# Optimization experiments

Measured on AMD Instinct MI355X. Metric: run time of the kernel, lower is better.

The kernel has to match this reference:

```python
import jax, jax.numpy as jnp
import numpy as np

B, G, P, D, H, QK, E, FF, TOPK = 32, 500, 500, 128, 8, 16, 8, 512, 2
SQRT_EMB = 11.313708498984761
LOGIT_CLIP = 10.0
EPS_CV = 1e-10
EPS_IN = 1e-5


def setup_inputs() -> dict:
    key = jax.random.key(0)
    ks = jax.random.split(key, 16)
    s = 0.05
    inp = {
        'graph': jax.random.normal(ks[0], (B, 1, D), jnp.float32),
        'capacity': jax.random.uniform(ks[1], (B, G), jnp.float32),
        'ninf_mask': jnp.zeros((B, G, P), jnp.float32),
        'encoded_nodes': jax.random.normal(ks[2], (B, P, D), jnp.float32),
        'Wq': jax.random.normal(ks[3], (D + 1, H * QK), jnp.float32) * s,
        'Wk': jax.random.normal(ks[4], (D, H * QK), jnp.float32) * s,
        'Wv': jax.random.normal(ks[5], (D, H * QK), jnp.float32) * s,
        'Wcomb': jax.random.normal(ks[6], (H * QK, D), jnp.float32) * s,
        'w_gate': jax.random.normal(ks[7], (D, E), jnp.float32) * s,
        'W1': jax.random.normal(ks[8], (E, D, FF), jnp.float32) * s,
        'b1': jnp.zeros((E, FF), jnp.float32),
        'W2': jax.random.normal(ks[9], (E, FF, D), jnp.float32) * s,
        'b2': jnp.zeros((E, D), jnp.float32),
        'norm_w': jnp.ones((D,), jnp.float32),
        'norm_b': jnp.zeros((D,), jnp.float32),
    }
    return inp


def _heads(x, h):
    b, n, _ = x.shape
    return x.reshape(b, n, h, -1).transpose(0, 2, 1, 3)  # [b,h,n,qk]


def reference(graph, capacity, ninf_mask, encoded_nodes, Wq, Wk, Wv, Wcomb,
              w_gate, W1, b1, W2, b2, norm_w, norm_b):
    # ---- set_kv ----
    k = _heads(encoded_nodes @ Wk, H)  # [B,H,P,QK]
    v = _heads(encoded_nodes @ Wv, H)

    # ---- query build ----
    input1 = jnp.broadcast_to(graph, (B, G, D))
    input_cat = jnp.concatenate([input1, capacity[:, :, None]], axis=2)  # [B,G,D+1]
    q = _heads(input_cat @ Wq, H)  # [B,H,G,QK]

    # ---- multi-head attention ----
    score = jnp.einsum('bhgq,bhpq->bhgp', q, k) / jnp.sqrt(jnp.float32(QK))
    score = score + ninf_mask[:, None, :, :]
    w = jax.nn.softmax(score, axis=3)
    out = jnp.einsum('bhgp,bhpq->bhgq', w, v)
    out_concat = out.transpose(0, 2, 1, 3).reshape(B, G, H * QK)
    mh_atten_out = out_concat @ Wcomb  # [B,G,D]

    # ---- MoE (top-k gating, eval mode) ----
    tokens = mh_atten_out.reshape(B * G, D)
    logits = tokens @ w_gate                     # [T,E]
    topv, topi = jax.lax.top_k(logits, TOPK)
    topg = jax.nn.softmax(topv, axis=-1)
    T = tokens.shape[0]
    gates = jnp.zeros((T, E), tokens.dtype).at[jnp.arange(T)[:, None], topi].set(topg)
    importance = gates.sum(axis=0)
    moed_loss = jnp.var(importance, ddof=1) / (jnp.mean(importance) ** 2 + EPS_CV)
    h = jax.nn.relu(jnp.einsum('td,edf->tef', tokens, W1) + b1)  # [T,E,FF]
    y = jnp.einsum('tef,efd->ted', h, W2) + b2                   # [T,E,D]
    moe_out = jnp.einsum('te,ted->td', gates, y).reshape(B, G, D)

    # ---- Add & InstanceNorm1d (normalize over group dim per channel) ----
    added = mh_atten_out + moe_out
    mu = jnp.mean(added, axis=1, keepdims=True)
    var = jnp.var(added, axis=1, keepdims=True)
    normed = (added - mu) * jax.lax.rsqrt(var + EPS_IN) * norm_w + norm_b

    # ---- single-head probs ----
    score2 = jnp.einsum('bgd,bpd->bgp', normed, encoded_nodes)
    score_clipped = LOGIT_CLIP * jnp.tanh(score2 / SQRT_EMB)
    probs = jax.nn.softmax(score_clipped + ninf_mask, axis=2)
    return probs, moed_loss
```

## Files before the change

kernel.cpp:

```cpp
#include <hip/hip_runtime.h>
#include <math.h>

#define NB 32
#define NG 500
#define NP 500
#define ND 128
#define NH 8
#define NQK 16
#define NE 8
#define NFF 512
#define NT 16000

typedef __attribute__((ext_vector_type(8))) short bf16x8;
typedef __attribute__((ext_vector_type(4))) float f32x4;

static __device__ __forceinline__ unsigned short f2bf(float f) {
  unsigned int u = __float_as_uint(f);
  unsigned int r = (u + 0x7FFFu + ((u >> 16) & 1u)) >> 16;
  return (unsigned short)r;
}
static __device__ __forceinline__ float bf2f(unsigned short h) {
  return __uint_as_float(((unsigned int)h) << 16);
}

__global__ __launch_bounds__(256) void k_kv(const float* __restrict__ enc,
                                            const float* __restrict__ Wk,
                                            const float* __restrict__ Wv,
                                            float* __restrict__ kbuf,
                                            float* __restrict__ vbuf) {
  int r0 = blockIdx.x * 32;
  int tid = threadIdx.x;
  __shared__ float encS[32][128];
  const float4* e4 = (const float4*)(enc + (size_t)r0 * 128);
  float4* s4 = (float4*)&encS[0][0];
#pragma unroll
  for (int i = 0; i < 4; i++) s4[tid + i * 256] = e4[tid + i * 256];
  __syncthreads();
  int cg = tid & 31, rg = tid >> 5;
  int c0 = cg * 8;
  const float* W0 = (c0 < 128) ? (Wk + c0) : (Wv + (c0 - 128));
  float acc[4][8] = {};
  for (int d = 0; d < 128; d++) {
    float a0 = encS[rg * 4 + 0][d];
    float a1 = encS[rg * 4 + 1][d];
    float a2 = encS[rg * 4 + 2][d];
    float a3 = encS[rg * 4 + 3][d];
    float4 wlo = *(const float4*)(W0 + d * 128);
    float4 whi = *(const float4*)(W0 + d * 128 + 4);
    float w[8] = {wlo.x, wlo.y, wlo.z, wlo.w, whi.x, whi.y, whi.z, whi.w};
#pragma unroll
    for (int j = 0; j < 8; j++) {
      acc[0][j] += a0 * w[j];
      acc[1][j] += a1 * w[j];
      acc[2][j] += a2 * w[j];
      acc[3][j] += a3 * w[j];
    }
  }
#pragma unroll
  for (int i = 0; i < 4; i++) {
    int r = r0 + rg * 4 + i;
    int b = r / 500;
    int p = r - b * 500;
    int cc = (c0 < 128) ? c0 : (c0 - 128);
    int h = cc >> 4, qk = cc & 15;
    float* dst = (c0 < 128 ? kbuf : vbuf) + ((size_t)(b * 8 + h) * 500 + p) * 16 + qk;
    *(float4*)dst = make_float4(acc[i][0], acc[i][1], acc[i][2], acc[i][3]);
    *(float4*)(dst + 4) = make_float4(acc[i][4], acc[i][5], acc[i][6], acc[i][7]);
  }
}

__global__ void k_graphq(const float* __restrict__ graph,
                         const float* __restrict__ Wq,
                         float* __restrict__ gq) {
  int b = blockIdx.x, j = threadIdx.x;
  float s = 0.f;
  for (int d = 0; d < 128; d++) s += graph[b * 128 + d] * Wq[d * 128 + j];
  gq[b * 128 + j] = s;
}

__global__ __launch_bounds__(256) void k_maskT(const float* __restrict__ mask,
                                               unsigned short* __restrict__ mT) {
  int b = blockIdx.z;
  int pt = blockIdx.x * 32, gt = blockIdx.y * 32;
  __shared__ float t[32][33];
  int tx = threadIdx.x & 31, ty = threadIdx.x >> 5;
#pragma unroll
  for (int i = 0; i < 32; i += 8) {
    int g = gt + ty + i, p = pt + tx;
    t[ty + i][tx] = (g < NG && p < NP) ? mask[((size_t)b * NG + g) * NP + p] : 0.f;
  }
  __syncthreads();
#pragma unroll
  for (int i = 0; i < 32; i += 8) {
    int p = pt + ty + i, g = gt + tx;
    if (p < NP && g < NG)
      mT[((size_t)b * NP + p) * NG + g] = f2bf(t[tx][ty + i]);
  }
}

__global__ __launch_bounds__(256) void k_encT(const float* __restrict__ enc,
                                              float* __restrict__ encT) {
  int b = blockIdx.z;
  int pt = blockIdx.x * 32, dt = blockIdx.y * 32;
  __shared__ float t[32][33];
  int tx = threadIdx.x & 31, ty = threadIdx.x >> 5;
#pragma unroll
  for (int i = 0; i < 32; i += 8) {
    int p = pt + ty + i, d = dt + tx;
    t[ty + i][tx] = (p < NP) ? enc[((size_t)b * NP + p) * ND + d] : 0.f;
  }
  __syncthreads();
#pragma unroll
  for (int i = 0; i < 32; i += 8) {
    int d = dt + ty + i, p = pt + tx;
    if (p < NP)
      encT[((size_t)b * ND + d) * NP + p] = t[tx][ty + i];
  }
}

__global__ __launch_bounds__(256) void k_attn(const float* __restrict__ kbuf,
                                              const float* __restrict__ vbuf,
                                              const float* __restrict__ capacity,
                                              const float* __restrict__ gq,
                                              const float* __restrict__ Wq,
                                              const unsigned short* __restrict__ mT,
                                              float* __restrict__ att) {
  int d = blockIdx.x;
  int xc = d & 7, kk = d >> 3;
  int b = ((kk >> 3) << 3) | xc;
  int h = kk & 7;
  int bh = b * 8 + h;
  int half = blockIdx.y;
  int tid = threadIdx.x;
  __shared__ float2 AB[NP];
  __shared__ float vsh[NP][16];
  const float4* vp = (const float4*)(vbuf + (size_t)bh * NP * 16);
  float4* v4 = (float4*)&vsh[0][0];
  for (int i = tid; i < NP * 4; i += 256) v4[i] = vp[i];
  float gqv[16], wql[16];
#pragma unroll
  for (int j = 0; j < 16; j++) {
    gqv[j] = gq[b * 128 + h * 16 + j];
    wql[j] = Wq[128 * 128 + h * 16 + j];
  }
  const float4* kp = (const float4*)(kbuf + (size_t)bh * NP * 16);
  for (int p = tid; p < NP; p += 256) {
    float4 k0 = kp[p * 4 + 0], k1 = kp[p * 4 + 1];
    float4 k2 = kp[p * 4 + 2], k3 = kp[p * 4 + 3];
    float kv[16] = {k0.x, k0.y, k0.z, k0.w, k1.x, k1.y, k1.z, k1.w,
                    k2.x, k2.y, k2.z, k2.w, k3.x, k3.y, k3.z, k3.w};
    float a = 0.f, bb = 0.f;
#pragma unroll
    for (int j = 0; j < 16; j++) { a += gqv[j] * kv[j]; bb += wql[j] * kv[j]; }
    AB[p] = make_float2(a * 0.25f, bb * 0.25f);
  }
  __syncthreads();
  if (tid < 250) {
    int g = half * 250 + tid;
    float cap = capacity[b * NG + g];
    float l = 0.f;
    float o[16] = {};
    const unsigned short* mTb = mT + (size_t)b * NP * NG + g;
    for (int p = 0; p < NP; p++) {
      float2 ab = AB[p];
      float mval = bf2f(mTb[(size_t)p * NG]);
      float e = __expf(fmaf(cap, ab.y, ab.x) + mval);
      l += e;
      const float4* vr = (const float4*)(&vsh[p][0]);
      float4 va = vr[0], vb = vr[1], vc = vr[2], vd = vr[3];
      o[0] += e * va.x;  o[1] += e * va.y;  o[2] += e * va.z;  o[3] += e * va.w;
      o[4] += e * vb.x;  o[5] += e * vb.y;  o[6] += e * vb.z;  o[7] += e * vb.w;
      o[8] += e * vc.x;  o[9] += e * vc.y;  o[10] += e * vc.z; o[11] += e * vc.w;
      o[12] += e * vd.x; o[13] += e * vd.y; o[14] += e * vd.z; o[15] += e * vd.w;
    }
    float inv = 1.f / l;
    float* orow = att + ((size_t)(b * NG + g)) * 128 + h * 16;
#pragma unroll
    for (int j = 0; j < 16; j++) orow[j] = o[j] * inv;
  }
}

__global__ __launch_bounds__(256) void k_comb(const float* __restrict__ att,
                                              const float* __restrict__ Wc,
                                              float* __restrict__ mh) {
  int r0 = blockIdx.x * 32;
  int tid = threadIdx.x;
  __shared__ float aS[32][130];
  for (int idx = tid; idx < 32 * 32; idx += 256) {
    int r = idx >> 5, dg = idx & 31;
    float4 v = ((const float4*)att)[(size_t)(r0 + r) * 32 + dg];
    aS[r][dg * 4 + 0] = v.x; aS[r][dg * 4 + 1] = v.y;
    aS[r][dg * 4 + 2] = v.z; aS[r][dg * 4 + 3] = v.w;
  }
  __syncthreads();
  int cg = tid & 15, rg = tid >> 4;
  float acc[2][8] = {};
  for (int d = 0; d < 128; d++) {
    float a0 = aS[rg * 2 + 0][d];
    float a1 = aS[rg * 2 + 1][d];
    float4 wlo = *(const float4*)(Wc + d * 128 + cg * 8);
    float4 whi = *(const float4*)(Wc + d * 128 + cg * 8 + 4);
    float w[8] = {wlo.x, wlo.y, wlo.z, wlo.w, whi.x, whi.y, whi.z, whi.w};
#pragma unroll
    for (int j = 0; j < 8; j++) {
      acc[0][j] += a0 * w[j];
      acc[1][j] += a1 * w[j];
    }
  }
#pragma unroll
  for (int i = 0; i < 2; i++) {
    float* dst = mh + (size_t)(r0 + rg * 2 + i) * 128 + cg * 8;
    *(float4*)dst = make_float4(acc[i][0], acc[i][1], acc[i][2], acc[i][3]);
    *(float4*)(dst + 4) = make_float4(acc[i][4], acc[i][5], acc[i][6], acc[i][7]);
  }
}

__global__ __launch_bounds__(256) void k_gate(const float* __restrict__ mh,
                                              const float* __restrict__ wg,
                                              int* __restrict__ tlist,
                                              float* __restrict__ glist,
                                              int* __restrict__ cnt,
                                              float* __restrict__ imp) {
  int t0 = blockIdx.x * 256;
  int tid = threadIdx.x;
  __shared__ float wgS[128 * 8];
  __shared__ int lcnt[8];
  __shared__ float limp[8];
  __shared__ int lbase[8];
  for (int i = tid; i < 1024; i += 256) wgS[i] = wg[i];
  if (tid < 8) { lcnt[tid] = 0; limp[tid] = 0.f; }
  __syncthreads();
  int t = t0 + tid;
  bool ok = (t < NT);
  int i0 = 0, i1 = 0, r0 = 0, r1 = 0;
  float g0 = 0.f, g1 = 0.f;
  if (ok) {
    float lg[8] = {};
    const float* row = mh + (size_t)t * ND;
    for (int d = 0; d < ND; d += 4) {
      float4 x4 = *(const float4*)(row + d);
      float xs[4] = {x4.x, x4.y, x4.z, x4.w};
#pragma unroll
      for (int u = 0; u < 4; u++)
#pragma unroll
        for (int k = 0; k < 8; k++) lg[k] += xs[u] * wgS[(d + u) * 8 + k];
    }
    float v0 = -1e30f, v1 = -1e30f;
#pragma unroll
    for (int k = 0; k < 8; k++) {
      float l = lg[k];
      if (l > v0) { v1 = v0; i1 = i0; v0 = l; i0 = k; }
      else if (l > v1) { v1 = l; i1 = k; }
    }
    float ex = __expf(v1 - v0);
    float den = 1.0f + ex;
    g0 = 1.0f / den; g1 = ex / den;
    atomicAdd(&limp[i0], g0);
    atomicAdd(&limp[i1], g1);
    r0 = atomicAdd(&lcnt[i0], 1);
    r1 = atomicAdd(&lcnt[i1], 1);
  }
  __syncthreads();
  if (tid < 8) {
    lbase[tid] = atomicAdd(&cnt[tid], lcnt[tid]);
    atomicAdd(&imp[tid], limp[tid]);
  }
  __syncthreads();
  if (ok) {
    int p0 = lbase[i0] + r0;
    tlist[i0 * NT + p0] = t; glist[i0 * NT + p0] = g0;
    int p1 = lbase[i1] + r1;
    tlist[i1 * NT + p1] = t; glist[i1 * NT + p1] = g1;
  }
}

__global__ __launch_bounds__(64) void k_wpack(const float* __restrict__ W1,
                                              const float* __restrict__ W2,
                                              unsigned short* __restrict__ w1h,
                                              unsigned short* __restrict__ w1l,
                                              unsigned short* __restrict__ w2h,
                                              unsigned short* __restrict__ w2l) {
  int bid = blockIdx.x;
  int e = bid >> 8;
  int t = bid & 255;
  int l = threadIdx.x;
  int kg = 4 * (l >> 4);
  if (t < 128) {
    int kt = t >> 5, nt = t & 31;
    const float* src = W1 + (size_t)e * 128 * 512;
    size_t base = ((((size_t)e * 4 + kt) * 32 + nt) * 64 + l) * 8;
    int n = nt * 16 + (l & 15);
#pragma unroll
    for (int j = 0; j < 8; j++) {
      int k = kt * 32 + kg + (j & 3) + ((j >> 2) << 4);
      float v = src[(size_t)k * 512 + n];
      unsigned short hi = f2bf(v);
      w1h[base + j] = hi;
      w1l[base + j] = f2bf(v - bf2f(hi));
    }
  } else {
    int tt = t - 128;
    int kt = tt >> 3, nt = tt & 7;
    const float* src = W2 + (size_t)e * 512 * 128;
    size_t base = ((((size_t)e * 16 + kt) * 8 + nt) * 64 + l) * 8;
    int n = nt * 16 + (l & 15);
#pragma unroll
    for (int j = 0; j < 8; j++) {
      int k = kt * 32 + kg + (j & 3) + ((j >> 2) << 4);
      float v = src[(size_t)k * 128 + n];
      unsigned short hi = f2bf(v);
      w2h[base + j] = hi;
      w2l[base + j] = f2bf(v - bf2f(hi));
    }
  }
}

__global__ __launch_bounds__(256) void k_moe(const float* __restrict__ mh,
                                             const unsigned short* __restrict__ w1h,
                                             const unsigned short* __restrict__ w1l,
                                             const unsigned short* __restrict__ w2h,
                                             const unsigned short* __restrict__ w2l,
                                             const float* __restrict__ b1,
                                             const float* __restrict__ b2,
                                             const int* __restrict__ tlist,
                                             const float* __restrict__ glist,
                                             const int* __restrict__ cnt,
                                             float* __restrict__ acc) {
  int e = blockIdx.y;
  int n = cnt[e];
  int t0 = blockIdx.x * 32;
  if (t0 >= n) return;
  int tid = threadIdx.x;
  int wq = tid >> 6;
  int l = tid & 63;
  __shared__ int rT[32];
  __shared__ float rG[32];
  __shared__ unsigned short hH[32][132];
  __shared__ unsigned short hL[32][132];
  if (tid < 32) {
    int ok = (t0 + tid) < n;
    rT[tid] = ok ? tlist[e * NT + t0 + tid] : -1;
    rG[tid] = ok ? glist[e * NT + t0 + tid] : 0.f;
  }
  __syncthreads();

  int kg = 4 * (l >> 4);
  bf16x8 Ah[2][4], Al[2][4];
#pragma unroll
  for (int m = 0; m < 2; m++) {
    int myrow = m * 16 + (l & 15);
    int mytok = rT[myrow];
#pragma unroll
    for (int kt = 0; kt < 4; kt++) {
      float v[8];
      if (mytok >= 0) {
        const float* row = mh + (size_t)mytok * ND + kt * 32 + kg;
        float4 a = *(const float4*)(row);
        float4 b = *(const float4*)(row + 16);
        v[0] = a.x; v[1] = a.y; v[2] = a.z; v[3] = a.w;
        v[4] = b.x; v[5] = b.y; v[6] = b.z; v[7] = b.w;
      } else {
#pragma unroll
        for (int j = 0; j < 8; j++) v[j] = 0.f;
      }
#pragma unroll
      for (int j = 0; j < 8; j++) {
        unsigned short hi = f2bf(v[j]);
        Ah[m][kt][j] = (short)hi;
        Al[m][kt][j] = (short)f2bf(v[j] - bf2f(hi));
      }
    }
  }

  f32x4 zero4 = {0.f, 0.f, 0.f, 0.f};
  f32x4 yB[2][2] = {{zero4, zero4}, {zero4, zero4}};

  for (int c = 0; c < 4; c++) {
    f32x4 accA[2][2] = {{zero4, zero4}, {zero4, zero4}};
#pragma unroll
    for (int kt = 0; kt < 4; kt++) {
      bf16x8 bh[2], bl[2];
#pragma unroll
      for (int nt = 0; nt < 2; nt++) {
        int ntg = c * 8 + wq * 2 + nt;
        size_t fo = ((((size_t)e * 4 + kt) * 32 + ntg) * 64 + l) * 8;
        bh[nt] = *(const bf16x8*)(w1h + fo);
        bl[nt] = *(const bf16x8*)(w1l + fo);
      }
#pragma unroll
      for (int nt = 0; nt < 2; nt++)
#pragma unroll
        for (int m = 0; m < 2; m++) {
          accA[m][nt] = __builtin_amdgcn_mfma_f32_16x16x32_bf16(Ah[m][kt], bh[nt], accA[m][nt], 0, 0, 0);
          accA[m][nt] = __builtin_amdgcn_mfma_f32_16x16x32_bf16(Ah[m][kt], bl[nt], accA[m][nt], 0, 0, 0);
          accA[m][nt] = __builtin_amdgcn_mfma_f32_16x16x32_bf16(Al[m][kt], bh[nt], accA[m][nt], 0, 0, 0);
        }
    }
    __syncthreads();
#pragma unroll
    for (int nt = 0; nt < 2; nt++) {
      int nloc = wq * 32 + nt * 16 + (l & 15);
      float bv = b1[e * NFF + c * 128 + nloc];
#pragma unroll
      for (int m = 0; m < 2; m++)
#pragma unroll
        for (int r = 0; r < 4; r++) {
          int row = m * 16 + (l >> 4) * 4 + r;
          float hv = fmaxf(accA[m][nt][r] + bv, 0.f);
          unsigned short hi = f2bf(hv);
          hH[row][nloc] = hi;
          hL[row][nloc] = f2bf(hv - bf2f(hi));
        }
    }
    __syncthreads();
#pragma unroll
    for (int kt = 0; kt < 4; kt++) {
      int kb = kt * 32 + kg;
      bf16x8 ah2[2], al2[2];
#pragma unroll
      for (int m = 0; m < 2; m++) {
        int r2 = m * 16 + (l & 15);
        union { unsigned long long u[2]; bf16x8 v; } ua, ub;
        ua.u[0] = *(const unsigned long long*)(&hH[r2][kb]);
        ua.u[1] = *(const unsigned long long*)(&hH[r2][kb + 16]);
        ub.u[0] = *(const unsigned long long*)(&hL[r2][kb]);
        ub.u[1] = *(const unsigned long long*)(&hL[r2][kb + 16]);
        ah2[m] = ua.v; al2[m] = ub.v;
      }
      bf16x8 wh[2], wl[2];
#pragma unroll
      for (int nt = 0; nt < 2; nt++) {
        int ntg = wq * 2 + nt;
        size_t fo = ((((size_t)e * 16 + (c * 4 + kt)) * 8 + ntg) * 64 + l) * 8;
        wh[nt] = *(const bf16x8*)(w2h + fo);
        wl[nt] = *(const bf16x8*)(w2l + fo);
      }
#pragma unroll
      for (int nt = 0; nt < 2; nt++)
#pragma unroll
        for (int m = 0; m < 2; m++) {
          yB[m][nt] = __builtin_amdgcn_mfma_f32_16x16x32_bf16(ah2[m], wh[nt], yB[m][nt], 0, 0, 0);
          yB[m][nt] = __builtin_amdgcn_mfma_f32_16x16x32_bf16(ah2[m], wl[nt], yB[m][nt], 0, 0, 0);
          yB[m][nt] = __builtin_amdgcn_mfma_f32_16x16x32_bf16(al2[m], wh[nt], yB[m][nt], 0, 0, 0);
        }
    }
  }
#pragma unroll
  for (int nt = 0; nt < 2; nt++) {
    int d = (wq * 2 + nt) * 16 + (l & 15);
    float b2v = b2[e * ND + d];
#pragma unroll
    for (int m = 0; m < 2; m++)
#pragma unroll
      for (int r = 0; r < 4; r++) {
        int row = m * 16 + (l >> 4) * 4 + r;
        int tok = rT[row];
        if (tok >= 0)
          atomicAdd(acc + (size_t)tok * ND + d, rG[row] * (yB[m][nt][r] + b2v));
      }
  }
}

__global__ void k_loss(const float* __restrict__ imp, float* __restrict__ out) {
  if (threadIdx.x == 0 && blockIdx.x == 0) {
    float s = 0.f;
    for (int k = 0; k < 8; k++) s += imp[k];
    float mu = s * 0.125f;
    float v = 0.f;
    for (int k = 0; k < 8; k++) { float d = imp[k] - mu; v += d * d; }
    v *= (1.0f / 7.0f);
    out[8000000] = v / (mu * mu + 1e-10f);
  }
}

__global__ __launch_bounds__(256) void k_norm(const float* __restrict__ mh,
                                              const float* __restrict__ moe,
                                              const float* __restrict__ nw,
                                              const float* __restrict__ nb,
                                              float* __restrict__ outn) {
  int b = blockIdx.y;
  int d0 = blockIdx.x * 16;
  int tid = threadIdx.x;
  int dl = tid & 15, gs = tid >> 4;
  int d = d0 + dl;
  float s1 = 0.f, s2 = 0.f;
  for (int g = gs; g < NG; g += 16) {
    int idx = (b * NG + g) * ND + d;
    float x = mh[idx] + moe[idx];
    s1 += x; s2 += x * x;
  }
  __shared__ float r1[16][17], r2[16][17];
  __shared__ float sw[16], sb[16];
  r1[gs][dl] = s1; r2[gs][dl] = s2;
  __syncthreads();
  if (gs == 0) {
    float a = 0.f, q = 0.f;
    for (int k = 0; k < 16; k++) { a += r1[k][dl]; q += r2[k][dl]; }
    float mu = a * (1.0f / NG);
    float var = q * (1.0f / NG) - mu * mu;
    float rs = rsqrtf(var + 1e-5f);
    float w = nw[d] * rs;
    sw[dl] = w;
    sb[dl] = nb[d] - mu * w;
  }
  __syncthreads();
  float w = sw[dl], bb = sb[dl];
  for (int g = gs; g < NG; g += 16) {
    int idx = (b * NG + g) * ND + d;
    float x = mh[idx] + moe[idx];
    outn[idx] = x * w + bb;
  }
}

__global__ __launch_bounds__(256) void k_probs(const float* __restrict__ normed,
                                               const float* __restrict__ encT,
                                               const float* __restrict__ mask,
                                               float* __restrict__ out) {
  int b = blockIdx.y;
  int g0 = blockIdx.x * 32;
  int tid = threadIdx.x;
  int gl = tid >> 3, pc = tid & 7;
  int g = g0 + gl;
  __shared__ float nS[32][130];
  __shared__ float eT[128][64];
  for (int idx = tid; idx < 32 * 32; idx += 256) {
    int r = idx >> 5, dg = idx & 31;
    int gg = g0 + r;
    float4 v = (gg < NG) ? ((const float4*)normed)[(size_t)(b * NG + gg) * 32 + dg]
                         : make_float4(0.f, 0.f, 0.f, 0.f);
    nS[r][dg * 4 + 0] = v.x; nS[r][dg * 4 + 1] = v.y;
    nS[r][dg * 4 + 2] = v.z; nS[r][dg * 4 + 3] = v.w;
  }
  float sc[8][8];
#pragma unroll
  for (int ch = 0; ch < 8; ch++) {
    int p0 = ch * 64;
    __syncthreads();
    for (int idx = tid; idx < 128 * 16; idx += 256) {
      int d = idx >> 4, c4 = idx & 15;
      int pp = p0 + c4 * 4;
      const float* src = encT + ((size_t)b * ND + d) * NP;
      float4 v;
      if (pp + 3 < NP) {
        v = *(const float4*)(src + pp);
      } else {
        v.x = (pp + 0 < NP) ? src[pp + 0] : 0.f;
        v.y = (pp + 1 < NP) ? src[pp + 1] : 0.f;
        v.z = (pp + 2 < NP) ? src[pp + 2] : 0.f;
        v.w = (pp + 3 < NP) ? src[pp + 3] : 0.f;
      }
      *(float4*)(&eT[d][c4 * 4]) = v;
    }
    __syncthreads();
    float a0 = 0, a1 = 0, a2 = 0, a3 = 0, a4 = 0, a5 = 0, a6 = 0, a7 = 0;
    for (int d = 0; d < 128; d++) {
      float nv = nS[gl][d];
      float4 e0 = *(const float4*)(&eT[d][pc * 8]);
      float4 e1 = *(const float4*)(&eT[d][pc * 8 + 4]);
      a0 += nv * e0.x; a1 += nv * e0.y; a2 += nv * e0.z; a3 += nv * e0.w;
      a4 += nv * e1.x; a5 += nv * e1.y; a6 += nv * e1.z; a7 += nv * e1.w;
    }
    sc[ch][0] = a0; sc[ch][1] = a1; sc[ch][2] = a2; sc[ch][3] = a3;
    sc[ch][4] = a4; sc[ch][5] = a5; sc[ch][6] = a6; sc[ch][7] = a7;
  }
  const float* mrow = mask + (size_t)(b * NG + (g < NG ? g : NG - 1)) * NP;
  float m = -1e30f;
#pragma unroll
  for (int ch = 0; ch < 8; ch++) {
#pragma unroll
    for (int j = 0; j < 8; j++) {
      int p = ch * 64 + pc * 8 + j;
      float v;
      if (p < NP) {
        float x = sc[ch][j] * (1.0f / 11.313708498984761f);
        float e2 = __expf(2.0f * x);
        float th = (e2 - 1.0f) / (e2 + 1.0f);
        v = 10.0f * th + mrow[p];
      } else {
        v = -1e30f;
      }
      sc[ch][j] = v;
      m = fmaxf(m, v);
    }
  }
  m = fmaxf(m, __shfl_xor(m, 1));
  m = fmaxf(m, __shfl_xor(m, 2));
  m = fmaxf(m, __shfl_xor(m, 4));
  float sum = 0.f;
#pragma unroll
  for (int ch = 0; ch < 8; ch++) {
#pragma unroll
    for (int j = 0; j < 8; j++) {
      float e = __expf(sc[ch][j] - m);
      sc[ch][j] = e;
      sum += e;
    }
  }
  sum += __shfl_xor(sum, 1);
  sum += __shfl_xor(sum, 2);
  sum += __shfl_xor(sum, 4);
  float inv = 1.0f / sum;
  if (g < NG) {
    float* orow = out + (size_t)(b * NG + g) * NP;
#pragma unroll
    for (int ch = 0; ch < 8; ch++) {
      int p = ch * 64 + pc * 8;
#pragma unroll
      for (int j = 0; j < 8; j++)
        if (p + j < NP) orow[p + j] = sc[ch][j] * inv;
    }
  }
}

extern "C" void kernel_launch(void* const* d_in, const int* in_sizes, int n_in,
                              void* d_out, int out_size, void* d_ws, size_t ws_size,
                              hipStream_t stream) {
  const float* graph    = (const float*)d_in[0];
  const float* capacity = (const float*)d_in[1];
  const float* mask     = (const float*)d_in[2];
  const float* enc      = (const float*)d_in[3];
  const float* Wq       = (const float*)d_in[4];
  const float* Wk       = (const float*)d_in[5];
  const float* Wv       = (const float*)d_in[6];
  const float* Wc       = (const float*)d_in[7];
  const float* wg       = (const float*)d_in[8];
  const float* W1       = (const float*)d_in[9];
  const float* b1       = (const float*)d_in[10];
  const float* W2       = (const float*)d_in[11];
  const float* b2       = (const float*)d_in[12];
  const float* nw       = (const float*)d_in[13];
  const float* nb       = (const float*)d_in[14];
  float* out = (float*)d_out;
  float* ws = (float*)d_ws;

  float* kbuf = ws;
  float* vbuf = ws + 2048000;
  float* att  = ws + 4096000;
  float* mh   = ws + 6144000;
  float* gq   = ws + 8192000;
  int*   tlist = (int*)(ws + 8196096);
  float* glist = ws + 8324096;
  int*   cnt  = (int*)(ws + 8452096);
  float* imp  = ws + 8452104;
  unsigned short* w1h = (unsigned short*)(ws + 8452112);
  unsigned short* w1l = (unsigned short*)(ws + 8714256);
  unsigned short* w2h = (unsigned short*)(ws + 8976400);
  unsigned short* w2l = (unsigned short*)(ws + 9238544);
  unsigned short* mT = (unsigned short*)(ws + 9500688);

  k_maskT<<<dim3(16, 16, 32), 256, 0, stream>>>(mask, mT);
  k_wpack<<<2048, 64, 0, stream>>>(W1, W2, w1h, w1l, w2h, w2l);
  k_kv<<<500, 256, 0, stream>>>(enc, Wk, Wv, kbuf, vbuf);
  k_graphq<<<32, 128, 0, stream>>>(graph, Wq, gq);
  k_attn<<<dim3(256, 2), 256, 0, stream>>>(kbuf, vbuf, capacity, gq, Wq, mT, att);
  hipMemsetAsync(kbuf, 0, 2048000 * sizeof(float), stream);
  hipMemsetAsync(cnt, 0, 64, stream);
  k_comb<<<500, 256, 0, stream>>>(att, Wc, mh);
  k_encT<<<dim3(16, 4, 32), 256, 0, stream>>>(enc, att);
  k_gate<<<63, 256, 0, stream>>>(mh, wg, tlist, glist, cnt, imp);
  k_moe<<<dim3(500, 8), 256, 0, stream>>>(mh, w1h, w1l, w2h, w2l, b1, b2,
                                          tlist, glist, cnt, kbuf);
  k_loss<<<1, 64, 0, stream>>>(imp, out);
  k_norm<<<dim3(8, 32), 256, 0, stream>>>(mh, kbuf, nw, nb, vbuf);
  k_probs<<<dim3(16, 32), 256, 0, stream>>>(vbuf, att, mask, out);
}
```

Baseline: 335.2 us.

## Compute probs score GEMM with split-bf16 MFMA using prepacked encoder fragments

Replaces the scalar FP32 shared-memory GEMM in k_probs with bf16x3 (hi/lo split) MFMA 16x16x32 instructions. The transpose kernel becomes a packer that writes encoded_nodes as hi/lo bf16 fragments in MFMA operand layout. Softmax drops the max subtraction because the logits are bounded by tanh clipping, and it reduces row sums across waves through shared memory. This trades exact FP32 accumulation for a three-term bf16 approximation and adds a second packed buffer.

```diff
diff --git a/kernel.cpp b/kernel.cpp
--- a/kernel.cpp
+++ b/kernel.cpp
@@ -98,23 +98,24 @@
   }
 }
 
-__global__ __launch_bounds__(256) void k_encT(const float* __restrict__ enc,
-                                              float* __restrict__ encT) {
-  int b = blockIdx.z;
-  int pt = blockIdx.x * 32, dt = blockIdx.y * 32;
-  __shared__ float t[32][33];
-  int tx = threadIdx.x & 31, ty = threadIdx.x >> 5;
-#pragma unroll
-  for (int i = 0; i < 32; i += 8) {
-    int p = pt + ty + i, d = dt + tx;
-    t[ty + i][tx] = (p < NP) ? enc[((size_t)b * NP + p) * ND + d] : 0.f;
-  }
-  __syncthreads();
-#pragma unroll
-  for (int i = 0; i < 32; i += 8) {
-    int d = dt + ty + i, p = pt + tx;
-    if (p < NP)
-      encT[((size_t)b * ND + d) * NP + p] = t[tx][ty + i];
+__global__ __launch_bounds__(64) void k_encpack(const float* __restrict__ enc,
+                                                unsigned short* __restrict__ eph,
+                                                unsigned short* __restrict__ epl) {
+  int bid = blockIdx.x;
+  int b = bid >> 7;
+  int t = bid & 127;
+  int kt = t >> 5, nt = t & 31;
+  int l = threadIdx.x;
+  int kg = 4 * (l >> 4);
+  int p = nt * 16 + (l & 15);
+  size_t base = ((((size_t)b * 4 + kt) * 32 + nt) * 64 + l) * 8;
+#pragma unroll
+  for (int j = 0; j < 8; j++) {
+    int k = kt * 32 + kg + (j & 3) + ((j >> 2) << 4);
+    float v = (p < NP) ? enc[((size_t)b * NP + p) * ND + k] : 0.f;
+    unsigned short hi = f2bf(v);
+    eph[base + j] = hi;
+    epl[base + j] = f2bf(v - bf2f(hi));
   }
 }
 
@@ -513,103 +514,128 @@
 }
 
 __global__ __launch_bounds__(256) void k_probs(const float* __restrict__ normed,
-                                               const float* __restrict__ encT,
+                                               const unsigned short* __restrict__ eph,
+                                               const unsigned short* __restrict__ epl,
                                                const float* __restrict__ mask,
                                                float* __restrict__ out) {
   int b = blockIdx.y;
   int g0 = blockIdx.x * 32;
   int tid = threadIdx.x;
-  int gl = tid >> 3, pc = tid & 7;
-  int g = g0 + gl;
-  __shared__ float nS[32][130];
-  __shared__ float eT[128][64];
-  for (int idx = tid; idx < 32 * 32; idx += 256) {
-    int r = idx >> 5, dg = idx & 31;
-    int gg = g0 + r;
-    float4 v = (gg < NG) ? ((const float4*)normed)[(size_t)(b * NG + gg) * 32 + dg]
-                         : make_float4(0.f, 0.f, 0.f, 0.f);
-    nS[r][dg * 4 + 0] = v.x; nS[r][dg * 4 + 1] = v.y;
-    nS[r][dg * 4 + 2] = v.z; nS[r][dg * 4 + 3] = v.w;
-  }
-  float sc[8][8];
-#pragma unroll
-  for (int ch = 0; ch < 8; ch++) {
-    int p0 = ch * 64;
-    __syncthreads();
-    for (int idx = tid; idx < 128 * 16; idx += 256) {
-      int d = idx >> 4, c4 = idx & 15;
-      int pp = p0 + c4 * 4;
-      const float* src = encT + ((size_t)b * ND + d) * NP;
-      float4 v;
-      if (pp + 3 < NP) {
-        v = *(const float4*)(src + pp);
+  int wq = tid >> 6;
+  int l = tid & 63;
+  int col = l & 15, lr = l >> 4;
+  int kg = 4 * lr;
+  __shared__ float ps[4][32];
+
+  bf16x8 Ah[2][4], Al[2][4];
+#pragma unroll
+  for (int m = 0; m < 2; m++) {
+    int g = g0 + m * 16 + col;
+#pragma unroll
+    for (int kt = 0; kt < 4; kt++) {
+      float v[8];
+      if (g < NG) {
+        const float* row = normed + ((size_t)b * NG + g) * ND + kt * 32 + kg;
+        float4 a = *(const float4*)(row);
+        float4 bb = *(const float4*)(row + 16);
+        v[0] = a.x; v[1] = a.y; v[2] = a.z; v[3] = a.w;
+        v[4] = bb.x; v[5] = bb.y; v[6] = bb.z; v[7] = bb.w;
       } else {
-        v.x = (pp + 0 < NP) ? src[pp + 0] : 0.f;
-        v.y = (pp + 1 < NP) ? src[pp + 1] : 0.f;
-        v.z = (pp + 2 < NP) ? src[pp + 2] : 0.f;
-        v.w = (pp + 3 < NP) ? src[pp + 3] : 0.f;
-      }
-      *(float4*)(&eT[d][c4 * 4]) = v;
-    }
-    __syncthreads();
-    float a0 = 0, a1 = 0, a2 = 0, a3 = 0, a4 = 0, a5 = 0, a6 = 0, a7 = 0;
-    for (int d = 0; d < 128; d++) {
-      float nv = nS[gl][d];
-      float4 e0 = *(const float4*)(&eT[d][pc * 8]);
-      float4 e1 = *(const float4*)(&eT[d][pc * 8 + 4]);
-      a0 += nv * e0.x; a1 += nv * e0.y; a2 += nv * e0.z; a3 += nv * e0.w;
-      a4 += nv * e1.x; a5 += nv * e1.y; a6 += nv * e1.z; a7 += nv * e1.w;
-    }
-    sc[ch][0] = a0; sc[ch][1] = a1; sc[ch][2] = a2; sc[ch][3] = a3;
-    sc[ch][4] = a4; sc[ch][5] = a5; sc[ch][6] = a6; sc[ch][7] = a7;
-  }
-  const float* mrow = mask + (size_t)(b * NG + (g < NG ? g : NG - 1)) * NP;
-  float m = -1e30f;
-#pragma unroll
-  for (int ch = 0; ch < 8; ch++) {
-#pragma unroll
-    for (int j = 0; j < 8; j++) {
-      int p = ch * 64 + pc * 8 + j;
-      float v;
-      if (p < NP) {
-        float x = sc[ch][j] * (1.0f / 11.313708498984761f);
+#pragma unroll
+        for (int j = 0; j < 8; j++) v[j] = 0.f;
+      }
+#pragma unroll
+      for (int j = 0; j < 8; j++) {
+        unsigned short hi = f2bf(v[j]);
+        Ah[m][kt][j] = (short)hi;
+        Al[m][kt][j] = (short)f2bf(v[j] - bf2f(hi));
+      }
+    }
+  }
+
+  f32x4 zero4 = {0.f, 0.f, 0.f, 0.f};
+  f32x4 acc[2][8];
+#pragma unroll
+  for (int m = 0; m < 2; m++)
+#pragma unroll
+    for (int nt = 0; nt < 8; nt++) acc[m][nt] = zero4;
+
+#pragma unroll
+  for (int kt = 0; kt < 4; kt++) {
+#pragma unroll
+    for (int nt = 0; nt < 8; nt++) {
+      int ntg = wq * 8 + nt;
+      size_t fo = ((((size_t)b * 4 + kt) * 32 + ntg) * 64 + l) * 8;
+      bf16x8 bh = *(const bf16x8*)(eph + fo);
+      bf16x8 bl = *(const bf16x8*)(epl + fo);
+#pragma unroll
+      for (int m = 0; m < 2; m++) {
+        acc[m][nt] = __builtin_amdgcn_mfma_f32_16x16x32_bf16(Ah[m][kt], bh, acc[m][nt], 0, 0, 0);
+        acc[m][nt] = __builtin_amdgcn_mfma_f32_16x16x32_bf16(Ah[m][kt], bl, acc[m][nt], 0, 0, 0);
+        acc[m][nt] = __builtin_amdgcn_mfma_f32_16x16x32_bf16(Al[m][kt], bh, acc[m][nt], 0, 0, 0);
+      }
+    }
+  }
+
+  float psum[2][4] = {};
+#pragma unroll
+  for (int m = 0; m < 2; m++)
+#pragma unroll
+    for (int nt = 0; nt < 8; nt++) {
+      int p = wq * 128 + nt * 16 + col;
+#pragma unroll
+      for (int r = 0; r < 4; r++) {
+        int g = g0 + m * 16 + 4 * lr + r;
+        float s = acc[m][nt][r];
+        float x = s * (1.0f / 11.313708498984761f);
         float e2 = __expf(2.0f * x);
         float th = (e2 - 1.0f) / (e2 + 1.0f);
-        v = 10.0f * th + mrow[p];
-      } else {
-        v = -1e30f;
-      }
-      sc[ch][j] = v;
-      m = fmaxf(m, v);
-    }
-  }
-  m = fmaxf(m, __shfl_xor(m, 1));
-  m = fmaxf(m, __shfl_xor(m, 2));
-  m = fmaxf(m, __shfl_xor(m, 4));
-  float sum = 0.f;
-#pragma unroll
-  for (int ch = 0; ch < 8; ch++) {
-#pragma unroll
-    for (int j = 0; j < 8; j++) {
-      float e = __expf(sc[ch][j] - m);
-      sc[ch][j] = e;
-      sum += e;
-    }
-  }
-  sum += __shfl_xor(sum, 1);
-  sum += __shfl_xor(sum, 2);
-  sum += __shfl_xor(sum, 4);
-  float inv = 1.0f / sum;
-  if (g < NG) {
-    float* orow = out + (size_t)(b * NG + g) * NP;
-#pragma unroll
-    for (int ch = 0; ch < 8; ch++) {
-      int p = ch * 64 + pc * 8;
-#pragma unroll
-      for (int j = 0; j < 8; j++)
-        if (p + j < NP) orow[p + j] = sc[ch][j] * inv;
-    }
-  }
+        float v;
+        if (p < NP && g < NG)
+          v = 10.0f * th + mask[((size_t)b * NG + g) * NP + p];
+        else
+          v = -1e30f;
+        float e = __expf(v);
+        acc[m][nt][r] = e;
+        psum[m][r] += e;
+      }
+    }
+#pragma unroll
+  for (int m = 0; m < 2; m++)
+#pragma unroll
+    for (int r = 0; r < 4; r++) {
+      float s = psum[m][r];
+      s += __shfl_xor(s, 1);
+      s += __shfl_xor(s, 2);
+      s += __shfl_xor(s, 4);
+      s += __shfl_xor(s, 8);
+      psum[m][r] = s;
+    }
+  if (col == 0) {
+#pragma unroll
+    for (int m = 0; m < 2; m++)
+#pragma unroll
+      for (int r = 0; r < 4; r++)
+        ps[wq][m * 16 + 4 * lr + r] = psum[m][r];
+  }
+  __syncthreads();
+#pragma unroll
+  for (int m = 0; m < 2; m++)
+#pragma unroll
+    for (int r = 0; r < 4; r++) {
+      int rowl = m * 16 + 4 * lr + r;
+      float tot = ps[0][rowl] + ps[1][rowl] + ps[2][rowl] + ps[3][rowl];
+      float inv = 1.0f / tot;
+      int g = g0 + rowl;
+      if (g < NG) {
+#pragma unroll
+        for (int nt = 0; nt < 8; nt++) {
+          int p = wq * 128 + nt * 16 + col;
+          if (p < NP)
+            out[((size_t)b * NG + g) * NP + p] = acc[m][nt][r] * inv;
+        }
+      }
+    }
 }
 
 extern "C" void kernel_launch(void* const* d_in, const int* in_sizes, int n_in,
@@ -647,6 +673,8 @@
   unsigned short* w2h = (unsigned short*)(ws + 8976400);
   unsigned short* w2l = (unsigned short*)(ws + 9238544);
   unsigned short* mT = (unsigned short*)(ws + 9500688);
+  unsigned short* eph = (unsigned short*)att;
+  unsigned short* epl = (unsigned short*)(ws + 13500688);
 
   k_maskT<<<dim3(16, 16, 32), 256, 0, stream>>>(mask, mT);
   k_wpack<<<2048, 64, 0, stream>>>(W1, W2, w1h, w1l, w2h, w2l);
@@ -656,11 +684,11 @@
   hipMemsetAsync(kbuf, 0, 2048000 * sizeof(float), stream);
   hipMemsetAsync(cnt, 0, 64, stream);
   k_comb<<<500, 256, 0, stream>>>(att, Wc, mh);
-  k_encT<<<dim3(16, 4, 32), 256, 0, stream>>>(enc, att);
+  k_encpack<<<4096, 64, 0, stream>>>(enc, eph, epl);
   k_gate<<<63, 256, 0, stream>>>(mh, wg, tlist, glist, cnt, imp);
   k_moe<<<dim3(500, 8), 256, 0, stream>>>(mh, w1h, w1l, w2h, w2l, b1, b2,
                                           tlist, glist, cnt, kbuf);
   k_loss<<<1, 64, 0, stream>>>(imp, out);
   k_norm<<<dim3(8, 32), 256, 0, stream>>>(mh, kbuf, nw, nb, vbuf);
-  k_probs<<<dim3(16, 32), 256, 0, stream>>>(vbuf, att, mask, out);
-}
+  k_probs<<<dim3(16, 32), 256, 0, stream>>>(vbuf, eph, epl, mask, out);
+}
```

Result: faster. 311.9 us (-7.0%).
